# Kernel tuning notes

Measured on AMD Instinct MI355X. Metric: run time of the kernel, lower is better.

Reference implementation:

```python
import jax, jax.numpy as jnp
import numpy as np

B, D = 8192, 1024
HR, HE, HF = 512, 4096, 2048
N_OPS, N_TASKS = 4, 4

def setup_inputs() -> dict:
    key = jax.random.key(0)
    ks = jax.random.split(key, 20)
    s = 0.02
    return {
        "x":        jax.random.normal(ks[0], (B, D), jnp.float32),
        # router
        "W_r1":   s*jax.random.normal(ks[1], (D, HR), jnp.float32),
        "b_r1":     jnp.zeros((HR,), jnp.float32),
        "W_dom":  s*jax.random.normal(ks[2], (HR, 2), jnp.float32),
        "b_dom":    jnp.zeros((2,), jnp.float32),
        "W_mop":  s*jax.random.normal(ks[3], (HR, N_OPS), jnp.float32),
        "W_lt":   s*jax.random.normal(ks[4], (HR, N_TASKS), jnp.float32),
        # math expert (operation hint = additive embedding)
        "op_emb": s*jax.random.normal(ks[5], (N_OPS, D), jnp.float32),
        "W_m1":   s*jax.random.normal(ks[6], (D, HE), jnp.float32),
        "b_m1":     jnp.zeros((HE,), jnp.float32),
        "W_m2":   s*jax.random.normal(ks[7], (HE, D), jnp.float32),
        "b_m2":     jnp.zeros((D,), jnp.float32),
        # language expert (task hint = additive embedding)
        "task_emb": s*jax.random.normal(ks[8], (N_TASKS, D), jnp.float32),
        "W_l1":   s*jax.random.normal(ks[9], (D, HE), jnp.float32),
        "b_l1":     jnp.zeros((HE,), jnp.float32),
        "W_l2":   s*jax.random.normal(ks[10], (HE, D), jnp.float32),
        "b_l2":     jnp.zeros((D,), jnp.float32),
        # fusion
        "W_f1":   s*jax.random.normal(ks[11], (D, HF), jnp.float32),
        "b_f1":     jnp.zeros((HF,), jnp.float32),
        "W_f2":   s*jax.random.normal(ks[12], (HF, D), jnp.float32),
        "b_f2":     jnp.zeros((D,), jnp.float32),
    }

def reference(x, W_r1, b_r1, W_dom, b_dom, W_mop, W_lt,
              op_emb, W_m1, b_m1, W_m2, b_m2,
              task_emb, W_l1, b_l1, W_l2, b_l2,
              W_f1, b_f1, W_f2, b_f2):
    # --- router ---
    h = jax.nn.relu(x @ W_r1 + b_r1)                      # [B, HR]
    dom_logits = h @ W_dom + b_dom                        # [B, 2]
    expert_weights = jax.nn.softmax(dom_logits, axis=-1)  # [B, 2]
    primary = jnp.argmax(dom_logits, axis=-1)             # [B]
    math_op = jnp.argmax(h @ W_mop, axis=-1)              # [B]
    lang_task = jnp.argmax(h @ W_lt, axis=-1)             # [B]
    # --- experts (vectorized equivalent of per-sample dispatch) ---
    math_in = x + op_emb[math_op]                         # [B, D]
    math_out = jax.nn.relu(math_in @ W_m1 + b_m1) @ W_m2 + b_m2
    lang_in = x + task_emb[lang_task]                     # [B, D]
    lang_out = jax.nn.relu(lang_in @ W_l1 + b_l1) @ W_l2 + b_l2
    selected = jnp.where((primary == 0)[:, None], math_out, lang_out)  # [B, D]
    # --- fusion: scale by routing weight of the chosen expert + MLP residual ---
    w = jnp.take_along_axis(expert_weights, primary[:, None], axis=1)  # [B, 1]
    fused = w * selected
    final = fused + jax.nn.relu(fused @ W_f1 + b_f1) @ W_f2 + b_f2     # [B, D]
    return final
```

## Files before the change

kernel.cpp:

```cpp
#include <hip/hip_runtime.h>
#include <hip/hip_bf16.h>
#include <stdint.h>

#define NB 8192
#define DD 1024
#define HRD 512
#define HED 4096
#define HFD 2048

typedef __attribute__((ext_vector_type(8))) short bf16x8;
typedef __attribute__((ext_vector_type(4))) float f32x4;
typedef unsigned short u16;

__device__ __forceinline__ u16 f2b(float f) {
    union { float f; uint32_t i; } c; c.f = f;
    uint32_t r = c.i + 0x7FFF + ((c.i >> 16) & 1);
    return (u16)(r >> 16);
}
__device__ __forceinline__ float b2f(u16 u) {
    union { uint32_t i; float f; } c; c.i = ((uint32_t)u) << 16; return c.f;
}

__device__ __forceinline__ void xcd_swz(int flat, int nwg, int nFast, int& f, int& s) {
    int xcd = flat & 7, rest = flat >> 3;
    int q = nwg >> 3, r = nwg & 7;
    int wg = (xcd < r ? xcd * (q + 1) : r * (q + 1) + (xcd - r) * q) + rest;
    f = wg % nFast; s = wg / nFast;
}

#define GLDS(g, l) __builtin_amdgcn_global_load_lds( \
    (const __attribute__((address_space(1))) void*)(g), \
    (__attribute__((address_space(3))) void*)(l), 16, 0, 0)

__global__ void k_init(int* cnt) { if (threadIdx.x < 2) cnt[threadIdx.x] = 0; }

__global__ __launch_bounds__(256) void k_split(const float4* __restrict__ x4,
                                               ushort4* __restrict__ hi4,
                                               ushort4* __restrict__ lo4) {
    int i = blockIdx.x * 256 + threadIdx.x;
    float4 v = x4[i];
    ushort4 h, l;
    h.x = f2b(v.x); l.x = f2b(v.x - b2f(h.x));
    h.y = f2b(v.y); l.y = f2b(v.y - b2f(h.y));
    h.z = f2b(v.z); l.z = f2b(v.z - b2f(h.z));
    h.w = f2b(v.w); l.w = f2b(v.w - b2f(h.w));
    hi4[i] = h; lo4[i] = l;
}

__global__ __launch_bounds__(256) void k_transpose(const float* __restrict__ in,
                                                   u16* __restrict__ out, int R, int C) {
    __shared__ float s[64][65];
    int tx = threadIdx.x & 63, ty = threadIdx.x >> 6;
    int c0 = blockIdx.x * 64, r0 = blockIdx.y * 64;
#pragma unroll
    for (int j = 0; j < 16; j++) { int r = ty + j * 4; s[r][tx] = in[(size_t)(r0 + r) * C + c0 + tx]; }
    __syncthreads();
#pragma unroll
    for (int j = 0; j < 16; j++) { int c = ty + j * 4; out[(size_t)(c0 + c) * R + r0 + tx] = f2b(s[tx][c]); }
}

__global__ __launch_bounds__(256) void k_transpose_split(const float* __restrict__ in,
                                                         u16* __restrict__ ohi, u16* __restrict__ olo,
                                                         int R, int C) {
    __shared__ float s[64][65];
    int tx = threadIdx.x & 63, ty = threadIdx.x >> 6;
    int c0 = blockIdx.x * 64, r0 = blockIdx.y * 64;
#pragma unroll
    for (int j = 0; j < 16; j++) { int r = ty + j * 4; s[r][tx] = in[(size_t)(r0 + r) * C + c0 + tx]; }
    __syncthreads();
#pragma unroll
    for (int j = 0; j < 16; j++) {
        int c = ty + j * 4;
        float v = s[tx][c];
        u16 h = f2b(v);
        ohi[(size_t)(c0 + c) * R + r0 + tx] = h;
        olo[(size_t)(c0 + c) * R + r0 + tx] = f2b(v - b2f(h));
    }
}

__device__ __forceinline__ void stage_tile(const char* gRowBase, long rowStrideBytes,
                                           u16* s, int tid) {
    int wave = tid >> 6, lane = tid & 63;
#pragma unroll
    for (int is = 0; is < 4; ++is) {
        int c = wave * 4 + is;
        int row = c * 8 + (lane >> 3);
        const char* g = gRowBase + (long)row * rowStrideBytes + (lane & 7) * 16;
        GLDS(g, (char*)s + c * 1024);
    }
}

__global__ __launch_bounds__(256) void k_router(const u16* __restrict__ Ah, const u16* __restrict__ Al,
                                                const u16* __restrict__ Bh, const u16* __restrict__ Bl,
                                                const float* __restrict__ bias, float* __restrict__ H) {
    __shared__ u16 sAh[2][128 * 64], sAl[2][128 * 64], sBh[2][128 * 64], sBl[2][128 * 64];
    int tid = threadIdx.x, lane = tid & 63, wave = tid >> 6;
    int flat = blockIdx.y * gridDim.x + blockIdx.x;
    int bm, bn;
    xcd_swz(flat, gridDim.x * gridDim.y, gridDim.x, bm, bn);
    f32x4 acc[4][4];
#pragma unroll
    for (int i = 0; i < 4; i++)
#pragma unroll
        for (int j = 0; j < 4; j++) acc[i][j] = (f32x4)0.f;
    int wm = (wave & 1) * 64, wn = (wave >> 1) * 64;
    const char* ahBase = (const char*)(Ah + (size_t)bm * 128 * DD);
    const char* alBase = (const char*)(Al + (size_t)bm * 128 * DD);
    const char* bhBase = (const char*)(Bh + (size_t)bn * 128 * DD);
    const char* blBase = (const char*)(Bl + (size_t)bn * 128 * DD);
    const int nk = DD / 64;
    stage_tile(ahBase, DD * 2, sAh[0], tid);
    stage_tile(alBase, DD * 2, sAl[0], tid);
    stage_tile(bhBase, DD * 2, sBh[0], tid);
    stage_tile(blBase, DD * 2, sBl[0], tid);
    asm volatile("s_waitcnt vmcnt(0)" ::: "memory");
    __builtin_amdgcn_s_barrier();
    int cur = 0;
    for (int it = 0; it < nk; ++it) {
        if (it + 1 < nk) {
            size_t ofs = (size_t)(it + 1) * 128;
            stage_tile(ahBase + ofs, DD * 2, sAh[cur ^ 1], tid);
            stage_tile(alBase + ofs, DD * 2, sAl[cur ^ 1], tid);
            stage_tile(bhBase + ofs, DD * 2, sBh[cur ^ 1], tid);
            stage_tile(blBase + ofs, DD * 2, sBl[cur ^ 1], tid);
        }
        const u16* pAh = sAh[cur]; const u16* pAl = sAl[cur];
        const u16* pBh = sBh[cur]; const u16* pBl = sBl[cur];
#pragma unroll
        for (int kk = 0; kk < 2; kk++) {
            int kofs = kk * 64 + (lane >> 4) * 16;
            bf16x8 vbh[4], vbl[4];
#pragma unroll
            for (int ni = 0; ni < 4; ni++) {
                int rB = (wn + ni * 16 + (lane & 15)) * 128 + kofs;
                vbh[ni] = *(const bf16x8*)((const char*)pBh + rB);
                vbl[ni] = *(const bf16x8*)((const char*)pBl + rB);
            }
#pragma unroll
            for (int mi = 0; mi < 4; mi++) {
                int rA = (wm + mi * 16 + (lane & 15)) * 128 + kofs;
                bf16x8 vah = *(const bf16x8*)((const char*)pAh + rA);
                bf16x8 val = *(const bf16x8*)((const char*)pAl + rA);
#pragma unroll
                for (int ni = 0; ni < 4; ni++) {
                    acc[mi][ni] = __builtin_amdgcn_mfma_f32_16x16x32_bf16(vah, vbh[ni], acc[mi][ni], 0, 0, 0);
                    acc[mi][ni] = __builtin_amdgcn_mfma_f32_16x16x32_bf16(vah, vbl[ni], acc[mi][ni], 0, 0, 0);
                    acc[mi][ni] = __builtin_amdgcn_mfma_f32_16x16x32_bf16(val, vbh[ni], acc[mi][ni], 0, 0, 0);
                }
            }
        }
        asm volatile("s_waitcnt vmcnt(0)" ::: "memory");
        __builtin_amdgcn_s_barrier();
        cur ^= 1;
    }
    int quad = lane >> 4, cl = lane & 15;
#pragma unroll
    for (int mi = 0; mi < 4; mi++)
#pragma unroll
        for (int r = 0; r < 4; r++) {
            int row = bm * 128 + wm + mi * 16 + quad * 4 + r;
#pragma unroll
            for (int ni = 0; ni < 4; ni++) {
                int col = bn * 128 + wn + ni * 16 + cl;
                float v = acc[mi][ni][r] + bias[col];
                H[(size_t)row * HRD + col] = fmaxf(v, 0.f);
            }
        }
}

__global__ __launch_bounds__(256) void k_heads(const float* __restrict__ H,
                                               const float* __restrict__ Wd, const float* __restrict__ bd,
                                               const float* __restrict__ Wm, const float* __restrict__ Wl,
                                               int* __restrict__ cnt, int* __restrict__ perm,
                                               float* __restrict__ wsc, int* __restrict__ eic) {
    int lane = threadIdx.x & 63, wave = threadIdx.x >> 6;
    int r = blockIdx.x * 4 + wave;
    const float4* h4 = (const float4*)(H + (size_t)r * HRD);
    float4 v0 = h4[lane * 2], v1 = h4[lane * 2 + 1];
    float hv[8] = {v0.x, v0.y, v0.z, v0.w, v1.x, v1.y, v1.z, v1.w};
    float a[10];
#pragma unroll
    for (int t = 0; t < 10; t++) a[t] = 0.f;
    int kbase = lane * 8;
#pragma unroll
    for (int j = 0; j < 8; j++) {
        int k = kbase + j;
        float h_ = hv[j];
        float2 wd = ((const float2*)Wd)[k];
        a[0] += h_ * wd.x; a[1] += h_ * wd.y;
        float4 wm = ((const float4*)Wm)[k];
        a[2] += h_ * wm.x; a[3] += h_ * wm.y; a[4] += h_ * wm.z; a[5] += h_ * wm.w;
        float4 wl = ((const float4*)Wl)[k];
        a[6] += h_ * wl.x; a[7] += h_ * wl.y; a[8] += h_ * wl.z; a[9] += h_ * wl.w;
    }
#pragma unroll
    for (int t = 0; t < 10; t++)
#pragma unroll
        for (int off = 32; off > 0; off >>= 1) a[t] += __shfl_down(a[t], off);
    if (lane == 0) {
        float d0 = a[0] + bd[0], d1 = a[1] + bd[1];
        int primary = (d1 > d0) ? 1 : 0;
        float w = 1.f / (1.f + expf(-fabsf(d0 - d1)));
        int mi = 0; float mv = a[2];
        if (a[3] > mv) { mv = a[3]; mi = 1; }
        if (a[4] > mv) { mv = a[4]; mi = 2; }
        if (a[5] > mv) { mv = a[5]; mi = 3; }
        int li = 0; float lv = a[6];
        if (a[7] > lv) { lv = a[7]; li = 1; }
        if (a[8] > lv) { lv = a[8]; li = 2; }
        int pos;
        if (a[9] > lv) { lv = a[9]; li = 3; }
        if (primary == 0) pos = atomicAdd(&cnt[0], 1);
        else              pos = NB - 1 - atomicAdd(&cnt[1], 1);
        perm[pos] = r; wsc[pos] = w; eic[pos] = (primary == 0) ? mi : li;
    }
}

__global__ __launch_bounds__(256) void k_gather(const float* __restrict__ x,
                                                const float* __restrict__ op_emb,
                                                const float* __restrict__ task_emb,
                                                const int* __restrict__ perm, const int* __restrict__ eic,
                                                const int* __restrict__ cnt, u16* __restrict__ xin) {
    int lane = threadIdx.x & 63, wave = threadIdx.x >> 6;
    int i = blockIdx.x * 4 + wave;
    int n0 = cnt[0];
    int r = perm[i];
    const float* emb = ((i >= n0) ? task_emb : op_emb) + (size_t)eic[i] * DD;
    const float4* x4 = (const float4*)(x + (size_t)r * DD);
    const float4* e4 = (const float4*)emb;
    ushort4* o4 = (ushort4*)(xin + (size_t)i * DD);
#pragma unroll
    for (int j = 0; j < 4; j++) {
        int idx = lane + j * 64;
        float4 xv = x4[idx], ev = e4[idx];
        ushort4 o;
        o.x = f2b(xv.x + ev.x); o.y = f2b(xv.y + ev.y);
        o.z = f2b(xv.z + ev.z); o.w = f2b(xv.w + ev.w);
        o4[idx] = o;
    }
}

template <int EPI, bool DUAL>
__global__ __launch_bounds__(512) void k_gemm8p(
    const u16* __restrict__ A, const u16* __restrict__ B0, const u16* __restrict__ B1,
    const float* __restrict__ bias0, const float* __restrict__ bias1,
    void* __restrict__ Out, int K, int N,
    const int* __restrict__ cnt, const float* __restrict__ wsel,
    const int* __restrict__ perm, const u16* __restrict__ resid) {
    __shared__ __align__(16) u16 sA[2][128 * 64];
    __shared__ __align__(16) u16 sB[2][128 * 64];
    const int tid = threadIdx.x, lane = tid & 63, wave = tid >> 6;
    int flat = blockIdx.y * gridDim.x + blockIdx.x;
    int t, bn;
    xcd_swz(flat, gridDim.x * gridDim.y, gridDim.x, t, bn);

    int n0 = 0, tile = t, storeLo = 0, storeHi = 0x7fffffff;
    const u16* Bt = B0; const float* bias = bias0;
    if constexpr (DUAL) {
        n0 = cnt[0];
        int tb = n0 >> 7;
        bool isMath = (t <= tb) && (t < 64);
        tile = isMath ? t : (t - 1);
        if (isMath) { storeLo = tile * 128; storeHi = n0 < storeLo + 128 ? n0 : storeLo + 128; }
        else        { storeHi = tile * 128 + 128; storeLo = n0 > tile * 128 ? n0 : tile * 128;
                      Bt = B1; bias = bias1; }
        if (storeLo >= storeHi) return;
    }

    f32x4 acc[4][2];
#pragma unroll
    for (int i = 0; i < 4; i++)
#pragma unroll
        for (int j = 0; j < 2; j++) acc[i][j] = (f32x4)0.f;

    const int wm = (wave & 1) * 64;
    const int wn = (wave >> 1) * 32;
    const int rl = lane & 15, q = lane >> 4, x7 = lane & 7;

    const long stride = (long)K * 2;
    const char* aBase = (const char*)A + (size_t)tile * 128 * stride;
    const char* bBase = (const char*)Bt + (size_t)bn * 128 * stride;
    const int rowInUnit = tid >> 3;
    const long srcOfs = (long)((tid & 7) ^ (rowInUnit & 7)) << 4;
    const int ldsWaveOfs = wave * 1024;

    auto STAGE = [&](int kt, int d) {
        long kofs = (long)kt * 128 + srcOfs;
#pragma unroll
        for (int i = 0; i < 2; i++)
            GLDS(aBase + (long)(i * 64 + rowInUnit) * stride + kofs,
                 (char*)&sA[d][0] + i * 8192 + ldsWaveOfs);
#pragma unroll
        for (int i = 0; i < 2; i++)
            GLDS(bBase + (long)(i * 64 + rowInUnit) * stride + kofs,
                 (char*)&sB[d][0] + i * 8192 + ldsWaveOfs);
    };

    STAGE(0, 0);
    const int nk = K >> 6;
    for (int k = 0; k < nk; ++k) {
        const int r_ = k & 1;
        if (k + 1 < nk) {
            STAGE(k + 1, r_ ^ 1);
            asm volatile("s_waitcnt vmcnt(4)" ::: "memory");
        } else {
            asm volatile("s_waitcnt vmcnt(0)" ::: "memory");
        }
        __builtin_amdgcn_s_barrier();
        const char* pA = (const char*)&sA[r_][0];
        const char* pB = (const char*)&sB[r_][0];
        bf16x8 vaA[2][2], vaB[2][2], vb0[2], vb1[2];
#pragma unroll
        for (int f = 0; f < 2; f++)
#pragma unroll
            for (int kk = 0; kk < 2; kk++)
                vaA[f][kk] = *(const bf16x8*)(pA + (wm + f * 16 + rl) * 128 + (((kk * 4 + q) ^ x7) << 4));
#pragma unroll
        for (int kk = 0; kk < 2; kk++)
            vb0[kk] = *(const bf16x8*)(pB + (wn + rl) * 128 + (((kk * 4 + q) ^ x7) << 4));
        __builtin_amdgcn_s_setprio(1);
#pragma unroll
        for (int f = 0; f < 2; f++)
#pragma unroll
            for (int kk = 0; kk < 2; kk++)
                acc[f][0] = __builtin_amdgcn_mfma_f32_16x16x32_bf16(vaA[f][kk], vb0[kk], acc[f][0], 0, 0, 0);
        __builtin_amdgcn_s_setprio(0);
#pragma unroll
        for (int kk = 0; kk < 2; kk++)
            vb1[kk] = *(const bf16x8*)(pB + (wn + 16 + rl) * 128 + (((kk * 4 + q) ^ x7) << 4));
        __builtin_amdgcn_s_setprio(1);
#pragma unroll
        for (int f = 0; f < 2; f++)
#pragma unroll
            for (int kk = 0; kk < 2; kk++)
                acc[f][1] = __builtin_amdgcn_mfma_f32_16x16x32_bf16(vaA[f][kk], vb1[kk], acc[f][1], 0, 0, 0);
        __builtin_amdgcn_s_setprio(0);
#pragma unroll
        for (int f = 0; f < 2; f++)
#pragma unroll
            for (int kk = 0; kk < 2; kk++)
                vaB[f][kk] = *(const bf16x8*)(pA + (wm + 32 + f * 16 + rl) * 128 + (((kk * 4 + q) ^ x7) << 4));
        __builtin_amdgcn_s_setprio(1);
#pragma unroll
        for (int f = 0; f < 2; f++)
#pragma unroll
            for (int kk = 0; kk < 2; kk++)
                acc[2 + f][1] = __builtin_amdgcn_mfma_f32_16x16x32_bf16(vaB[f][kk], vb1[kk], acc[2 + f][1], 0, 0, 0);
        __builtin_amdgcn_s_setprio(0);
        __builtin_amdgcn_s_setprio(1);
#pragma unroll
        for (int f = 0; f < 2; f++)
#pragma unroll
            for (int kk = 0; kk < 2; kk++)
                acc[2 + f][0] = __builtin_amdgcn_mfma_f32_16x16x32_bf16(vaB[f][kk], vb0[kk], acc[2 + f][0], 0, 0, 0);
        __builtin_amdgcn_s_setprio(0);
        asm volatile("" ::: "memory");
        __builtin_amdgcn_s_barrier();
    }

    const int quad = lane >> 4, cl = lane & 15;
#pragma unroll
    for (int mi = 0; mi < 4; mi++)
#pragma unroll
        for (int r = 0; r < 4; r++) {
            int grow = tile * 128 + wm + mi * 16 + quad * 4 + r;
            if constexpr (DUAL) { if (grow < storeLo || grow >= storeHi) continue; }
#pragma unroll
            for (int ni = 0; ni < 2; ni++) {
                int col = bn * 128 + wn + ni * 16 + cl;
                float v = acc[mi][ni][r] + bias[col];
                if constexpr (EPI == 0) {
                    ((u16*)Out)[(size_t)grow * N + col] = f2b(fmaxf(v, 0.f));
                } else if constexpr (EPI == 1) {
                    ((u16*)Out)[(size_t)grow * N + col] = f2b(v * wsel[grow]);
                } else {
                    v += b2f(resid[(size_t)grow * N + col]);
                    ((float*)Out)[(size_t)perm[grow] * N + col] = v;
                }
            }
        }
}

extern "C" void kernel_launch(void* const* d_in, const int* in_sizes, int n_in,
                              void* d_out, int out_size, void* d_ws, size_t ws_size,
                              hipStream_t stream) {
    const float* x      = (const float*)d_in[0];
    const float* W_r1   = (const float*)d_in[1];
    const float* b_r1   = (const float*)d_in[2];
    const float* W_dom  = (const float*)d_in[3];
    const float* b_dom  = (const float*)d_in[4];
    const float* W_mop  = (const float*)d_in[5];
    const float* W_lt   = (const float*)d_in[6];
    const float* op_emb = (const float*)d_in[7];
    const float* W_m1   = (const float*)d_in[8];
    const float* b_m1   = (const float*)d_in[9];
    const float* W_m2   = (const float*)d_in[10];
    const float* b_m2   = (const float*)d_in[11];
    const float* task_emb = (const float*)d_in[12];
    const float* W_l1   = (const float*)d_in[13];
    const float* b_l1   = (const float*)d_in[14];
    const float* W_l2   = (const float*)d_in[15];
    const float* b_l2   = (const float*)d_in[16];
    const float* W_f1   = (const float*)d_in[17];
    const float* b_f1   = (const float*)d_in[18];
    const float* W_f2   = (const float*)d_in[19];
    const float* b_f2   = (const float*)d_in[20];

    char* wsp = (char*)d_ws;
    size_t off = 0;
    auto take = [&](size_t bytes) -> char* {
        char* p = wsp + off;
        off += (bytes + 255) & ~(size_t)255;
        return p;
    };
    u16* Wr_hi = (u16*)take((size_t)HRD * DD * 2);
    u16* Wr_lo = (u16*)take((size_t)HRD * DD * 2);
    u16* Wm1t  = (u16*)take((size_t)HED * DD * 2);
    u16* Wl1t  = (u16*)take((size_t)HED * DD * 2);
    u16* Wm2t  = (u16*)take((size_t)DD * HED * 2);
    u16* Wl2t  = (u16*)take((size_t)DD * HED * 2);
    u16* Wf1t  = (u16*)take((size_t)HFD * DD * 2);
    u16* Wf2t  = (u16*)take((size_t)DD * HFD * 2);
    u16* x_hi  = (u16*)take((size_t)NB * DD * 2);
    u16* x_lo  = (u16*)take((size_t)NB * DD * 2);
    float* Hbuf = (float*)take((size_t)NB * HRD * 4);
    u16* hid   = (u16*)take((size_t)NB * HED * 2);
    int* cnt   = (int*)take(256);
    int* perm  = (int*)take(NB * 4);
    int* eic   = (int*)take(NB * 4);
    float* wsc = (float*)take(NB * 4);
    u16* xin   = x_hi;
    u16* fused = x_lo;
    u16* hid2  = Wm1t;

    k_init<<<1, 64, 0, stream>>>(cnt);
    k_split<<<(NB * DD / 4) / 256, 256, 0, stream>>>((const float4*)x, (ushort4*)x_hi, (ushort4*)x_lo);
    k_transpose_split<<<dim3(HRD / 64, DD / 64), 256, 0, stream>>>(W_r1, Wr_hi, Wr_lo, DD, HRD);
    k_transpose<<<dim3(HED / 64, DD / 64), 256, 0, stream>>>(W_m1, Wm1t, DD, HED);
    k_transpose<<<dim3(HED / 64, DD / 64), 256, 0, stream>>>(W_l1, Wl1t, DD, HED);
    k_transpose<<<dim3(DD / 64, HED / 64), 256, 0, stream>>>(W_m2, Wm2t, HED, DD);
    k_transpose<<<dim3(DD / 64, HED / 64), 256, 0, stream>>>(W_l2, Wl2t, HED, DD);
    k_transpose<<<dim3(HFD / 64, DD / 64), 256, 0, stream>>>(W_f1, Wf1t, DD, HFD);
    k_transpose<<<dim3(DD / 64, HFD / 64), 256, 0, stream>>>(W_f2, Wf2t, HFD, DD);

    k_router<<<dim3(NB / 128, HRD / 128), 256, 0, stream>>>(x_hi, x_lo, Wr_hi, Wr_lo, b_r1, Hbuf);
    k_heads<<<NB / 4, 256, 0, stream>>>(Hbuf, W_dom, b_dom, W_mop, W_lt, cnt, perm, wsc, eic);
    k_gather<<<NB / 4, 256, 0, stream>>>(x, op_emb, task_emb, perm, eic, cnt, xin);

    k_gemm8p<0, true><<<dim3(NB / 128 + 1, HED / 128), 512, 0, stream>>>(
        xin, Wm1t, Wl1t, b_m1, b_l1, hid, DD, HED, cnt, nullptr, nullptr, nullptr);
    k_gemm8p<1, true><<<dim3(NB / 128 + 1, DD / 128), 512, 0, stream>>>(
        hid, Wm2t, Wl2t, b_m2, b_l2, fused, HED, DD, cnt, wsc, nullptr, nullptr);
    k_gemm8p<0, false><<<dim3(NB / 128, HFD / 128), 512, 0, stream>>>(
        fused, Wf1t, nullptr, b_f1, nullptr, hid2, DD, HFD, cnt, nullptr, nullptr, nullptr);
    k_gemm8p<2, false><<<dim3(NB / 128, DD / 128), 512, 0, stream>>>(
        hid2, Wf2t, nullptr, b_f2, nullptr, d_out, HFD, DD, cnt, nullptr, perm, fused);
}
```

Measured before the change: 686.9 us.

## Add 256x256-tile bf16 GEMM kernel for the up-projection layers

Measured after the change: 691.2 us. No clear change (+0.6%).

```diff
diff --git a/kernel.cpp b/kernel.cpp
--- a/kernel.cpp
+++ b/kernel.cpp
@@ -238,6 +238,150 @@
         o.z = f2b(xv.z + ev.z); o.w = f2b(xv.w + ev.w);
         o4[idx] = o;
     }
+}
+
+template <bool DUAL>
+__global__ __launch_bounds__(512) void k_g256(
+    const u16* __restrict__ A, const u16* __restrict__ B0w, const u16* __restrict__ B1w,
+    const float* __restrict__ bias0, const float* __restrict__ bias1,
+    u16* __restrict__ Out, int K, int N, const int* __restrict__ cnt) {
+    __shared__ __align__(16) u16 sA[2][256 * 64];
+    __shared__ __align__(16) u16 sB[2][256 * 64];
+    const int tid = threadIdx.x, lane = tid & 63, wave = tid >> 6;
+    int flat = blockIdx.y * gridDim.x + blockIdx.x;
+    int t, bn;
+    xcd_swz(flat, gridDim.x * gridDim.y, gridDim.x, t, bn);
+
+    int tile = t, storeLo = 0, storeHi = 0x7fffffff;
+    const u16* Bt = B0w; const float* bias = bias0;
+    if constexpr (DUAL) {
+        int n0 = cnt[0];
+        int tb = n0 >> 8;
+        bool isMath = (t <= tb) && (t < NB / 256);
+        tile = isMath ? t : (t - 1);
+        if (isMath) { storeLo = tile * 256; storeHi = n0 < storeLo + 256 ? n0 : storeLo + 256; }
+        else        { storeHi = tile * 256 + 256; storeLo = n0 > tile * 256 ? n0 : tile * 256;
+                      Bt = B1w; bias = bias1; }
+        if (storeLo >= storeHi) return;
+    }
+
+    f32x4 acc[8][4];
+#pragma unroll
+    for (int i = 0; i < 8; i++)
+#pragma unroll
+        for (int j = 0; j < 4; j++) acc[i][j] = (f32x4)0.f;
+
+    const int wm = (wave & 1) * 128;
+    const int wn = (wave >> 1) * 64;
+    const int rl = lane & 15, q = lane >> 4, x7 = lane & 7;
+
+    const long stride = (long)K * 2;
+    const char* aBase = (const char*)A + (size_t)tile * 256 * stride;
+    const char* bBase = (const char*)Bt + (size_t)bn * 256 * stride;
+    const int rowInUnit = tid >> 3;
+    const long srcOfs = (long)((tid & 7) ^ (rowInUnit & 7)) << 4;
+    const int waveOfs = wave * 1024;
+
+    auto SH = [&](const char* gBase, u16* ldsArr, int h, int kt) {
+        long kofs = (long)kt * 128 + srcOfs;
+#pragma unroll
+        for (int i = 0; i < 2; i++)
+            GLDS(gBase + (long)(h * 128 + i * 64 + rowInUnit) * stride + kofs,
+                 (char*)ldsArr + h * 16384 + i * 8192 + waveOfs);
+    };
+    auto STAGEF = [&](int kt, int d) {
+        SH(aBase, sA[d], 0, kt); SH(aBase, sA[d], 1, kt);
+        SH(bBase, sB[d], 0, kt); SH(bBase, sB[d], 1, kt);
+    };
+
+    const int nk = K >> 6;
+    STAGEF(0, 0);
+    bf16x8 va[4][2], vb0[2][2], vb1[2][2];
+    for (int kt = 0; kt < nk; ++kt) {
+        const int cur = kt & 1;
+        if (kt + 1 < nk) {
+            STAGEF(kt + 1, cur ^ 1);
+            asm volatile("s_waitcnt vmcnt(8)" ::: "memory");
+        } else {
+            asm volatile("s_waitcnt vmcnt(0)" ::: "memory");
+        }
+        __builtin_amdgcn_s_barrier();
+        const char* pA = (const char*)&sA[cur][0];
+        const char* pB = (const char*)&sB[cur][0];
+#pragma unroll
+        for (int f = 0; f < 4; f++)
+#pragma unroll
+            for (int kk = 0; kk < 2; kk++)
+                va[f][kk] = *(const bf16x8*)(pA + (wm + f * 16 + rl) * 128 + (((kk * 4 + q) ^ x7) << 4));
+#pragma unroll
+        for (int g = 0; g < 2; g++)
+#pragma unroll
+            for (int kk = 0; kk < 2; kk++)
+                vb0[g][kk] = *(const bf16x8*)(pB + (wn + g * 16 + rl) * 128 + (((kk * 4 + q) ^ x7) << 4));
+        __builtin_amdgcn_s_setprio(1);
+#pragma unroll
+        for (int f = 0; f < 4; f++)
+#pragma unroll
+            for (int g = 0; g < 2; g++)
+#pragma unroll
+                for (int kk = 0; kk < 2; kk++)
+                    acc[f][g] = __builtin_amdgcn_mfma_f32_16x16x32_bf16(va[f][kk], vb0[g][kk], acc[f][g], 0, 0, 0);
+        __builtin_amdgcn_s_setprio(0);
+#pragma unroll
+        for (int g = 0; g < 2; g++)
+#pragma unroll
+            for (int kk = 0; kk < 2; kk++)
+                vb1[g][kk] = *(const bf16x8*)(pB + (wn + 32 + g * 16 + rl) * 128 + (((kk * 4 + q) ^ x7) << 4));
+        __builtin_amdgcn_s_setprio(1);
+#pragma unroll
+        for (int f = 0; f < 4; f++)
+#pragma unroll
+            for (int g = 0; g < 2; g++)
+#pragma unroll
+                for (int kk = 0; kk < 2; kk++)
+                    acc[f][2 + g] = __builtin_amdgcn_mfma_f32_16x16x32_bf16(va[f][kk], vb1[g][kk], acc[f][2 + g], 0, 0, 0);
+        __builtin_amdgcn_s_setprio(0);
+#pragma unroll
+        for (int f = 0; f < 4; f++)
+#pragma unroll
+            for (int kk = 0; kk < 2; kk++)
+                va[f][kk] = *(const bf16x8*)(pA + (wm + 64 + f * 16 + rl) * 128 + (((kk * 4 + q) ^ x7) << 4));
+        __builtin_amdgcn_s_setprio(1);
+#pragma unroll
+        for (int f = 0; f < 4; f++)
+#pragma unroll
+            for (int g = 0; g < 2; g++)
+#pragma unroll
+                for (int kk = 0; kk < 2; kk++)
+                    acc[4 + f][2 + g] = __builtin_amdgcn_mfma_f32_16x16x32_bf16(va[f][kk], vb1[g][kk], acc[4 + f][2 + g], 0, 0, 0);
+        __builtin_amdgcn_s_setprio(0);
+        __builtin_amdgcn_s_setprio(1);
+#pragma unroll
+        for (int f = 0; f < 4; f++)
+#pragma unroll
+            for (int g = 0; g < 2; g++)
+#pragma unroll
+                for (int kk = 0; kk < 2; kk++)
+                    acc[4 + f][g] = __builtin_amdgcn_mfma_f32_16x16x32_bf16(va[f][kk], vb0[g][kk], acc[4 + f][g], 0, 0, 0);
+        __builtin_amdgcn_s_setprio(0);
+        asm volatile("" ::: "memory");
+        __builtin_amdgcn_s_barrier();
+    }
+
+    const int quad = lane >> 4, cl = lane & 15;
+#pragma unroll
+    for (int f = 0; f < 8; f++)
+#pragma unroll
+        for (int rr = 0; rr < 4; rr++) {
+            int grow = tile * 256 + wm + f * 16 + quad * 4 + rr;
+            if constexpr (DUAL) { if (grow < storeLo || grow >= storeHi) continue; }
+#pragma unroll
+            for (int g = 0; g < 4; g++) {
+                int col = bn * 256 + wn + g * 16 + cl;
+                float v = acc[f][g][rr] + bias[col];
+                Out[(size_t)grow * N + col] = f2b(fmaxf(v, 0.f));
+            }
+        }
 }
 
 template <int EPI, bool DUAL>
@@ -447,12 +591,12 @@
     k_heads<<<NB / 4, 256, 0, stream>>>(Hbuf, W_dom, b_dom, W_mop, W_lt, cnt, perm, wsc, eic);
     k_gather<<<NB / 4, 256, 0, stream>>>(x, op_emb, task_emb, perm, eic, cnt, xin);
 
-    k_gemm8p<0, true><<<dim3(NB / 128 + 1, HED / 128), 512, 0, stream>>>(
-        xin, Wm1t, Wl1t, b_m1, b_l1, hid, DD, HED, cnt, nullptr, nullptr, nullptr);
+    k_g256<true><<<dim3(NB / 256 + 1, HED / 256), 512, 0, stream>>>(
+        xin, Wm1t, Wl1t, b_m1, b_l1, hid, DD, HED, cnt);
     k_gemm8p<1, true><<<dim3(NB / 128 + 1, DD / 128), 512, 0, stream>>>(
         hid, Wm2t, Wl2t, b_m2, b_l2, fused, HED, DD, cnt, wsc, nullptr, nullptr);
-    k_gemm8p<0, false><<<dim3(NB / 128, HFD / 128), 512, 0, stream>>>(
-        fused, Wf1t, nullptr, b_f1, nullptr, hid2, DD, HFD, cnt, nullptr, nullptr, nullptr);
+    k_g256<false><<<dim3(NB / 256, HFD / 256), 512, 0, stream>>>(
+        fused, Wf1t, nullptr, b_f1, nullptr, hid2, DD, HFD, cnt);
     k_gemm8p<2, false><<<dim3(NB / 128, DD / 128), 512, 0, stream>>>(
         hid2, Wf2t, nullptr, b_f2, nullptr, d_out, HFD, DD, cnt, nullptr, perm, fused);
 }
```
